# Kernel tuning notes

Hardware: AMD Instinct MI355X
Metric: run time of the kernel (lower is better)

Reference implementation:

```python
import jax, jax.numpy as jnp
import numpy as np

N = 500_000
E = 8_000_000
IN, HID, OUT = 1, 10, 4
BN_EPS = 1e-5


def _lin_init(key, fan_in, fan_out):
    kw, kb = jax.random.split(key)
    s = 1.0 / np.sqrt(fan_in)
    W = jax.random.uniform(kw, (fan_in, fan_out), minval=-s, maxval=s, dtype=jnp.float32)
    b = jax.random.uniform(kb, (fan_out,), minval=-s, maxval=s, dtype=jnp.float32)
    return W, b


def setup_inputs() -> dict:
    key = jax.random.key(0)
    ks = jax.random.split(key, 12)
    x = jax.random.normal(ks[0], (N, IN), dtype=jnp.float32)
    edge_index = jax.random.randint(ks[1], (2, E), 0, N, dtype=jnp.int64)
    edge_attr = jax.random.uniform(ks[2], (E,), dtype=jnp.float32)
    inp = {"x": x, "edge_index": edge_index, "edge_attr": edge_attr}
    dims = [(IN, HID), (HID, HID), (HID, HID)]
    for i, (di, do) in enumerate(dims, start=1):
        k1, k2 = jax.random.split(ks[2 + i])
        W1, b1 = _lin_init(k1, di, do)
        W2, b2 = _lin_init(k2, do, do)
        inp[f"W{i}a"], inp[f"b{i}a"] = W1, b1
        inp[f"W{i}b"], inp[f"b{i}b"] = W2, b2
        inp[f"g{i}"] = jnp.ones((do,), jnp.float32)
        inp[f"be{i}"] = jnp.zeros((do,), jnp.float32)
    Wf, bf = _lin_init(ks[10], 3 * HID, OUT)
    inp["Wf"], inp["bf"] = Wf, bf
    return inp


def _gin_layer(x, src, dst, Wa, ba, Wb, bb, g, be):
    # GINConv (eps=0): h_i = MLP(x_i + sum_{j->i} x_j); Linear->Linear->BatchNorm (train mode)
    agg = jax.ops.segment_sum(x[src], dst, num_segments=N)  # [N, d]
    h = x + agg
    h = h @ Wa + ba
    h = h @ Wb + bb
    mu = jnp.mean(h, axis=0)
    var = jnp.var(h, axis=0)
    return g * (h - mu) * jax.lax.rsqrt(var + BN_EPS) + be


def _modularity(s, src, dst, w):
    two_m = jnp.sum(w)
    pos = jnp.sum(w * jnp.sum(s[src] * s[dst], axis=-1)) / two_m
    deg = jax.ops.segment_sum(w, src, num_segments=N)  # [N]
    ds = (deg @ s) / two_m  # [OUT]
    return pos - jnp.sum(ds * ds)


def reference(x, edge_index, edge_attr,
              W1a, b1a, W1b, b1b, g1, be1,
              W2a, b2a, W2b, b2b, g2, be2,
              W3a, b3a, W3b, b3b, g3, be3,
              Wf, bf):
    src, dst = edge_index[0], edge_index[1]
    x11 = _gin_layer(x, src, dst, W1a, b1a, W1b, b1b, g1, be1)
    x12 = _gin_layer(x11, src, dst, W2a, b2a, W2b, b2b, g2, be2)
    x13 = _gin_layer(x12, src, dst, W3a, b3a, W3b, b3b, g3, be3)
    logits = jnp.concatenate([x11, x12, x13], axis=-1) @ Wf + bf
    s = jax.nn.softmax(logits, axis=-1)
    q = _modularity(s, src, dst, edge_attr)
    return s, q
```

## Files before the change

### kernel.cpp

```cpp
#include <hip/hip_runtime.h>
#include <hip/hip_bf16.h>

#define NN 500000
#define NE 8000000
#define NB 123
#define BSH 12
#define BSZ 4096
#define CAP 69632
#define M 8
#define NAGG (NB * M)
#define BN_EPS 1e-5f

typedef unsigned uv4 __attribute__((ext_vector_type(4)));
typedef float fv4 __attribute__((ext_vector_type(4)));
typedef unsigned long long u64;

__device__ __forceinline__ float waveReduceF(float v) {
#pragma unroll
    for (int o = 32; o > 0; o >>= 1) v += __shfl_down(v, o, 64);
    return v;
}
__device__ __forceinline__ double waveReduceD(double v) {
#pragma unroll
    for (int o = 32; o > 0; o >>= 1) v += __shfl_down(v, o, 64);
    return v;
}
__device__ __forceinline__ float u2f(unsigned short u) {
    return __bfloat162float(__builtin_bit_cast(__hip_bfloat16, u));
}
__device__ __forceinline__ unsigned short f2u(float f) {
    return __builtin_bit_cast(unsigned short, __float2bfloat16(f));
}
__device__ __forceinline__ u64 pk1(float v) {
    int iv = (int)rintf(v * 268435456.f);
    return ((u64)(long long)iv << 20) + 1ull;
}

__global__ void initk(int* __restrict__ cur)
{
    if (threadIdx.x < NB) cur[threadIdx.x] = (int)threadIdx.x * CAP;
}

__global__ __launch_bounds__(512) void scatterk(
    const int4* __restrict__ src4, const int4* __restrict__ dst4,
    const float4* __restrict__ w4, int* __restrict__ cur,
    unsigned* __restrict__ pairs, unsigned short* __restrict__ wp)
{
    __shared__ unsigned sEnt[4096];
    __shared__ unsigned short sW[4096];
    __shared__ unsigned char sB[4096];
    __shared__ int h[8][128];
    __shared__ int wOff[8][128];
    __shared__ int bOff[128];
    __shared__ int lb[128];
    __shared__ int tot[128];

    int tid = threadIdx.x, wv = tid >> 6;
    for (int j = tid; j < 8 * 128; j += 512) (&h[0][0])[j] = 0;
    __syncthreads();

    unsigned en[8]; unsigned short wb[8]; int rb[8];
#pragma unroll
    for (int k = 0; k < 2; k++) {
        int q = blockIdx.x * 1024 + k * 512 + tid;
        if (q < NE / 4) {
            int4 s4 = src4[q]; int4 d4 = dst4[q]; float4 ww = w4[q];
            int ss[4] = {s4.x, s4.y, s4.z, s4.w};
            int dd[4] = {d4.x, d4.y, d4.z, d4.w};
            float fw[4] = {ww.x, ww.y, ww.z, ww.w};
#pragma unroll
            for (int i = 0; i < 4; i++) {
                int d = dd[i], b = d >> BSH;
                en[k * 4 + i] = ((unsigned)(d & (BSZ - 1)) << 19) | (unsigned)ss[i];
                wb[k * 4 + i] = f2u(fw[i]);
                int rk = atomicAdd(&h[wv][b], 1);
                rb[k * 4 + i] = (rk << 8) | b;
            }
        } else {
#pragma unroll
            for (int i = 0; i < 4; i++) rb[k * 4 + i] = -1;
        }
    }
    __syncthreads();
    if (tid < NB) {
        int acc = 0;
#pragma unroll
        for (int w = 0; w < 8; w++) { wOff[w][tid] = acc; acc += h[w][tid]; }
        tot[tid] = acc;
        lb[tid] = atomicAdd(&cur[tid], acc);
    }
    __syncthreads();
    if (tid == 0) {
        int acc = 0;
        for (int b = 0; b < NB; b++) { bOff[b] = acc; acc += tot[b]; }
    }
    __syncthreads();
#pragma unroll
    for (int k = 0; k < 8; k++) {
        if (rb[k] >= 0) {
            int b = rb[k] & 255, rk = rb[k] >> 8;
            int pos = bOff[b] + wOff[wv][b] + rk;
            sEnt[pos] = en[k]; sW[pos] = wb[k]; sB[pos] = (unsigned char)b;
        }
    }
    __syncthreads();
    int nE = NE - blockIdx.x * 4096; if (nE > 4096) nE = 4096;
    for (int j = tid; j < nE; j += 512) {
        int b = sB[j];
        int glob = lb[b] + (j - bOff[b]);
        pairs[glob] = sEnt[j];
        wp[glob] = sW[j];
    }
}

__global__ __launch_bounds__(512) void agg1k(
    const unsigned* __restrict__ pairs, const int* __restrict__ cur,
    const float* __restrict__ x, u64* __restrict__ slab)
{
    __shared__ u64 t[BSZ];
    for (int j = threadIdx.x; j < BSZ; j += 512) t[j] = 0ull;
    __syncthreads();
    int B = blockIdx.x / M, sl = blockIdx.x % M;
    int b0 = B * CAP;
    int len = cur[B] - b0;
    int seg = (((len + M - 1) / M) + 3) & ~3;
    int lo = b0 + sl * seg;
    int hi = lo + seg, e1 = b0 + len;
    if (hi > e1) hi = e1;
    int n = hi - lo;
    if (n > 0) {
        int nq = n >> 2;
        const uv4* pq = (const uv4*)(pairs + lo);
        for (int i = threadIdx.x; i < nq; i += 1024) {
            uv4 pA = __builtin_nontemporal_load(pq + i);
            int iB = i + 512;
            bool vB = iB < nq;
            float a0 = x[pA.x & 524287u];
            float a1 = x[pA.y & 524287u];
            float a2 = x[pA.z & 524287u];
            float a3 = x[pA.w & 524287u];
            float c0, c1, c2, c3; unsigned d4, d5, d6, d7;
            if (vB) {
                uv4 pB = __builtin_nontemporal_load(pq + iB);
                c0 = x[pB.x & 524287u]; d4 = pB.x >> 19;
                c1 = x[pB.y & 524287u]; d5 = pB.y >> 19;
                c2 = x[pB.z & 524287u]; d6 = pB.z >> 19;
                c3 = x[pB.w & 524287u]; d7 = pB.w >> 19;
            }
            atomicAdd(&t[pA.x >> 19], pk1(a0));
            atomicAdd(&t[pA.y >> 19], pk1(a1));
            atomicAdd(&t[pA.z >> 19], pk1(a2));
            atomicAdd(&t[pA.w >> 19], pk1(a3));
            if (vB) {
                atomicAdd(&t[d4], pk1(c0));
                atomicAdd(&t[d5], pk1(c1));
                atomicAdd(&t[d6], pk1(c2));
                atomicAdd(&t[d7], pk1(c3));
            }
        }
        int rem = n & 3;
        if ((int)threadIdx.x < rem) {
            unsigned p = pairs[lo + (nq << 2) + threadIdx.x];
            atomicAdd(&t[p >> 19], pk1(x[p & 524287u]));
        }
    }
    __syncthreads();
    u64* sb = slab + (size_t)blockIdx.x * BSZ;
    for (int j = threadIdx.x; j < BSZ; j += 512)
        __builtin_nontemporal_store(t[j], sb + j);
}

__global__ __launch_bounds__(256) void mergeN1(
    const u64* __restrict__ slab, const float* __restrict__ x,
    float2* __restrict__ UN2, u64* __restrict__ ENC)
{
    int i = blockIdx.x * 256 + threadIdx.x;
    if (i >= NN) return;
    int B = i >> BSH, low = i & (BSZ - 1);
    u64 s = 0ull;
#pragma unroll
    for (int m = 0; m < M; m++)
        s += __builtin_nontemporal_load(slab + (size_t)(B * M + m) * BSZ + low);
    unsigned cn = (unsigned)(s & 0xFFFFFull);
    long long sv = (long long)(s - (u64)cn) >> 20;
    float u = x[i] + (float)((double)sv * 3.725290298461914e-09);
    UN2[i] = make_float2(u, (float)cn);
    long long iu = (long long)rintf(u * 67108864.f);
    ENC[i] = ((u64)iu << 22) + (u64)cn;
}

__global__ __launch_bounds__(512) void agg2k(
    const unsigned* __restrict__ pairs, const int* __restrict__ cur,
    const u64* __restrict__ ENC, u64* __restrict__ slab)
{
    __shared__ u64 t[BSZ];
    for (int j = threadIdx.x; j < BSZ; j += 512) t[j] = 0ull;
    __syncthreads();
    int B = blockIdx.x / M, sl = blockIdx.x % M;
    int b0 = B * CAP;
    int len = cur[B] - b0;
    int seg = (((len + M - 1) / M) + 3) & ~3;
    int lo = b0 + sl * seg;
    int hi = lo + seg, e1 = b0 + len;
    if (hi > e1) hi = e1;
    int n = hi - lo;
    if (n > 0) {
        int nq = n >> 2;
        const uv4* pq = (const uv4*)(pairs + lo);
        for (int i = threadIdx.x; i < nq; i += 1024) {
            uv4 pA = __builtin_nontemporal_load(pq + i);
            int iB = i + 512;
            bool vB = iB < nq;
            u64 e0 = ENC[pA.x & 524287u];
            u64 e1v = ENC[pA.y & 524287u];
            u64 e2 = ENC[pA.z & 524287u];
            u64 e3 = ENC[pA.w & 524287u];
            u64 e4, e5, e6, e7; unsigned d4, d5, d6, d7;
            if (vB) {
                uv4 pB = __builtin_nontemporal_load(pq + iB);
                e4 = ENC[pB.x & 524287u]; d4 = pB.x >> 19;
                e5 = ENC[pB.y & 524287u]; d5 = pB.y >> 19;
                e6 = ENC[pB.z & 524287u]; d6 = pB.z >> 19;
                e7 = ENC[pB.w & 524287u]; d7 = pB.w >> 19;
            }
            atomicAdd(&t[pA.x >> 19], e0);
            atomicAdd(&t[pA.y >> 19], e1v);
            atomicAdd(&t[pA.z >> 19], e2);
            atomicAdd(&t[pA.w >> 19], e3);
            if (vB) {
                atomicAdd(&t[d4], e4);
                atomicAdd(&t[d5], e5);
                atomicAdd(&t[d6], e6);
                atomicAdd(&t[d7], e7);
            }
        }
        int rem = n & 3;
        if ((int)threadIdx.x < rem) {
            unsigned p = pairs[lo + (nq << 2) + threadIdx.x];
            atomicAdd(&t[p >> 19], ENC[p & 524287u]);
        }
    }
    __syncthreads();
    u64* sb = slab + (size_t)blockIdx.x * BSZ;
    for (int j = threadIdx.x; j < BSZ; j += 512)
        __builtin_nontemporal_store(t[j], sb + j);
}

__global__ __launch_bounds__(256) void mergeN2(
    const u64* __restrict__ slab, float* __restrict__ SU, float* __restrict__ SN)
{
    int i = blockIdx.x * 256 + threadIdx.x;
    if (i >= NN) return;
    int B = i >> BSH, low = i & (BSZ - 1);
    u64 s = 0ull;
#pragma unroll
    for (int m = 0; m < M; m++)
        s += __builtin_nontemporal_load(slab + (size_t)(B * M + m) * BSZ + low);
    unsigned sn = (unsigned)(s & 0x3FFFFFull);
    long long sv = (long long)(s - (u64)sn) >> 22;
    float su = (float)((double)sv * 1.4901161193847656e-08);
    SU[i] = su;
    SN[i] = (float)sn;
}

__global__ __launch_bounds__(512) void agg3k(
    const unsigned* __restrict__ pairs, const int* __restrict__ cur,
    const float* __restrict__ SU, float* __restrict__ slab)
{
    __shared__ float t[BSZ];
    for (int j = threadIdx.x; j < BSZ; j += 512) t[j] = 0.f;
    __syncthreads();
    int B = blockIdx.x / M, sl = blockIdx.x % M;
    int b0 = B * CAP;
    int len = cur[B] - b0;
    int seg = (((len + M - 1) / M) + 3) & ~3;
    int lo = b0 + sl * seg;
    int hi = lo + seg, e1 = b0 + len;
    if (hi > e1) hi = e1;
    int n = hi - lo;
    if (n > 0) {
        int nq = n >> 2;
        const uv4* pq = (const uv4*)(pairs + lo);
        for (int i = threadIdx.x; i < nq; i += 1024) {
            uv4 pA = __builtin_nontemporal_load(pq + i);
            int iB = i + 512;
            bool vB = iB < nq;
            float a0 = SU[pA.x & 524287u];
            float a1 = SU[pA.y & 524287u];
            float a2 = SU[pA.z & 524287u];
            float a3 = SU[pA.w & 524287u];
            float c0, c1, c2, c3; unsigned d4, d5, d6, d7;
            if (vB) {
                uv4 pB = __builtin_nontemporal_load(pq + iB);
                c0 = SU[pB.x & 524287u]; d4 = pB.x >> 19;
                c1 = SU[pB.y & 524287u]; d5 = pB.y >> 19;
                c2 = SU[pB.z & 524287u]; d6 = pB.z >> 19;
                c3 = SU[pB.w & 524287u]; d7 = pB.w >> 19;
            }
            atomicAdd(&t[pA.x >> 19], a0);
            atomicAdd(&t[pA.y >> 19], a1);
            atomicAdd(&t[pA.z >> 19], a2);
            atomicAdd(&t[pA.w >> 19], a3);
            if (vB) {
                atomicAdd(&t[d4], c0);
                atomicAdd(&t[d5], c1);
                atomicAdd(&t[d6], c2);
                atomicAdd(&t[d7], c3);
            }
        }
        int rem = n & 3;
        if ((int)threadIdx.x < rem) {
            unsigned p = pairs[lo + (nq << 2) + threadIdx.x];
            atomicAdd(&t[p >> 19], SU[p & 524287u]);
        }
    }
    __syncthreads();
    float* sb = slab + (size_t)blockIdx.x * BSZ;
    for (int j = threadIdx.x; j < BSZ; j += 512)
        __builtin_nontemporal_store(t[j], sb + j);
}

__global__ __launch_bounds__(256) void m3mom(
    const float* __restrict__ slab, const float2* __restrict__ UN2,
    const float* __restrict__ SU, const float* __restrict__ SN,
    float* __restrict__ SSU, double* __restrict__ dm)
{
    int i = blockIdx.x * 256 + threadIdx.x;
    double z[5] = {0, 0, 0, 0, 0};
    if (i < NN) {
        int B = i >> BSH, low = i & (BSZ - 1);
        float ssu = 0.f;
#pragma unroll
        for (int m = 0; m < M; m++)
            ssu += __builtin_nontemporal_load(slab + (size_t)(B * M + m) * BSZ + low);
        SSU[i] = ssu;
        float2 un = UN2[i];
        z[0] = (double)un.x; z[1] = (double)un.y; z[2] = (double)SU[i];
        z[3] = (double)SN[i]; z[4] = (double)ssu;
    }
    double m[20];
#pragma unroll
    for (int a = 0; a < 5; a++) m[a] = z[a];
    int idx = 5;
#pragma unroll
    for (int a = 0; a < 5; a++)
#pragma unroll
        for (int b = a; b < 5; b++) m[idx++] = z[a] * z[b];

    __shared__ double part[4][20];
    int lane = threadIdx.x & 63, wid = threadIdx.x >> 6;
#pragma unroll
    for (int k = 0; k < 20; k++) {
        double r = waveReduceD(m[k]);
        if (lane == 0) part[wid][k] = r;
    }
    __syncthreads();
    if (threadIdx.x < 20)
        atomicAdd(&dm[threadIdx.x],
                  part[0][threadIdx.x] + part[1][threadIdx.x] +
                  part[2][threadIdx.x] + part[3][threadIdx.x]);
}

__device__ void mm1010(const float* in, const float* Wa, const float* Wb, float* out)
{
    float t[10];
    for (int m = 0; m < 10; m++) {
        float acc = 0.f;
        for (int k = 0; k < 10; k++) acc += in[k] * Wa[k * 10 + m];
        t[m] = acc;
    }
    for (int j = 0; j < 10; j++) {
        float acc = 0.f;
        for (int m = 0; m < 10; m++) acc += t[m] * Wb[m * 10 + j];
        out[j] = acc;
    }
}

__global__ void constk(
    const float* __restrict__ W1a, const float* __restrict__ b1a,
    const float* __restrict__ W1b, const float* __restrict__ b1b,
    const float* __restrict__ g1, const float* __restrict__ be1,
    const float* __restrict__ W2a, const float* __restrict__ b2a,
    const float* __restrict__ W2b, const float* __restrict__ b2b,
    const float* __restrict__ g2, const float* __restrict__ be2,
    const float* __restrict__ W3a, const float* __restrict__ b3a,
    const float* __restrict__ W3b, const float* __restrict__ b3b,
    const float* __restrict__ g3, const float* __restrict__ be3,
    const float* __restrict__ Wf, const float* __restrict__ bf_,
    const double* __restrict__ dm, float* __restrict__ Lout)
{
    if (threadIdx.x != 0 || blockIdx.x != 0) return;
    const double invN = 1.0 / (double)NN;
    double E[5];
    for (int m = 0; m < 5; m++) E[m] = dm[m] * invN;
    double C[5][5];
    {
        int idx = 5;
        for (int a = 0; a < 5; a++)
            for (int b = a; b < 5; b++) {
                double c = dm[idx++] * invN - E[a] * E[b];
                C[a][b] = c; C[b][a] = c;
            }
    }
    float v[10], c1[10];
    for (int j = 0; j < 10; j++) {
        float av = 0.f, ac = 0.f;
        for (int k = 0; k < 10; k++) {
            av += W1a[k] * W1b[k * 10 + j];
            ac += b1a[k] * W1b[k * 10 + j];
        }
        v[j] = av; c1[j] = ac + b1b[j];
    }
    double Eu = E[0], Vu = C[0][0];
    float p[10], q[10];
    for (int j = 0; j < 10; j++) {
        float var1 = (float)(Vu * (double)v[j] * (double)v[j]);
        float sc1 = g1[j] * rsqrtf(var1 + BN_EPS);
        p[j] = sc1 * v[j];
        q[j] = be1[j] - (float)Eu * p[j];
    }
    float r[10], s[10], d2[10];
    mm1010(p, W2a, W2b, r);
    mm1010(q, W2a, W2b, s);
    for (int j = 0; j < 10; j++) {
        float acc = b2b[j];
        for (int m = 0; m < 10; m++) acc += b2a[m] * W2b[m * 10 + j];
        d2[j] = acc;
    }
    double Ea = E[0] + E[2], Eb = 1.0 + E[1];
    double Va = C[0][0] + 2.0 * C[0][2] + C[2][2];
    double Vb = C[1][1];
    double Cab = C[0][1] + C[2][1];
    float rt[10], st[10], dt[10];
    for (int j = 0; j < 10; j++) {
        double rj = r[j], sj = s[j];
        float var2 = (float)(Va * rj * rj + Vb * sj * sj + 2.0 * Cab * rj * sj);
        float sc2 = g2[j] * rsqrtf(var2 + BN_EPS);
        rt[j] = sc2 * r[j];
        st[j] = sc2 * s[j];
        dt[j] = be2[j] - sc2 * (float)(Ea * rj + Eb * sj);
    }
    float r3[10], s3[10], t3[10], d3[10];
    mm1010(rt, W3a, W3b, r3);
    mm1010(st, W3a, W3b, s3);
    mm1010(dt, W3a, W3b, t3);
    for (int j = 0; j < 10; j++) {
        float acc = b3b[j];
        for (int m = 0; m < 10; m++) acc += b3a[m] * W3b[m * 10 + j];
        d3[j] = acc;
    }
    const double gA[5] = {1, 0, 2, 0, 1};
    const double gB[5] = {0, 2, 0, 1, 0};
    const double gC[5] = {0, 1, 0, 0, 0};
    double EA = E[0] + 2.0 * E[2] + E[4];
    double EB = 1.0 + 2.0 * E[1] + E[3];
    double EC = 1.0 + E[1];
    double VA = 0, VB = 0, VC = 0, CAB = 0, CAC = 0, CBC = 0;
    for (int a = 0; a < 5; a++)
        for (int b = 0; b < 5; b++) {
            double c = C[a][b];
            VA  += gA[a] * gA[b] * c;
            VB  += gB[a] * gB[b] * c;
            VC  += gC[a] * gC[b] * c;
            CAB += gA[a] * gB[b] * c;
            CAC += gA[a] * gC[b] * c;
            CBC += gB[a] * gC[b] * c;
        }
    float rh[10], sh[10], th[10], dh[10];
    for (int j = 0; j < 10; j++) {
        double rj = r3[j], sj = s3[j], tj = t3[j];
        float var3 = (float)(VA * rj * rj + VB * sj * sj + VC * tj * tj
                             + 2.0 * (CAB * rj * sj + CAC * rj * tj + CBC * sj * tj));
        float sc3 = g3[j] * rsqrtf(var3 + BN_EPS);
        rh[j] = sc3 * r3[j];
        sh[j] = sc3 * s3[j];
        th[j] = sc3 * t3[j];
        dh[j] = be3[j] - sc3 * (float)(EA * rj + EB * sj + EC * tj);
    }
    for (int k = 0; k < 4; k++) {
        float Lu = 0, Ln = 0, Lsu = 0, Lsn = 0, Lssu = 0, L0 = bf_[k];
        for (int j = 0; j < 10; j++) {
            float wf1 = Wf[j * 4 + k];
            float wf2 = Wf[(10 + j) * 4 + k];
            float wf3 = Wf[(20 + j) * 4 + k];
            Lu   += p[j] * wf1 + rt[j] * wf2 + rh[j] * wf3;
            Ln   += st[j] * wf2 + (2.f * sh[j] + th[j]) * wf3;
            Lsu  += rt[j] * wf2 + 2.f * rh[j] * wf3;
            Lsn  += sh[j] * wf3;
            Lssu += rh[j] * wf3;
            L0   += q[j] * wf1 + (st[j] + dt[j]) * wf2 + (sh[j] + th[j] + dh[j]) * wf3;
        }
        Lout[0 * 4 + k] = Lu;  Lout[1 * 4 + k] = Ln;   Lout[2 * 4 + k] = Lsu;
        Lout[3 * 4 + k] = Lsn; Lout[4 * 4 + k] = Lssu; Lout[5 * 4 + k] = L0;
    }
}

__global__ __launch_bounds__(256) void finalk(
    const float2* __restrict__ UN2, const float* __restrict__ SU,
    const float* __restrict__ SN, const float* __restrict__ SSU,
    const float* __restrict__ L,
    float4* __restrict__ sout, ushort4* __restrict__ sbf)
{
    __shared__ float sL[24];
    if (threadIdx.x < 24) sL[threadIdx.x] = L[threadIdx.x];
    __syncthreads();
    int i = blockIdx.x * 256 + threadIdx.x;
    if (i >= NN) return;
    float2 un = UN2[i];
    float u = un.x, n = un.y, su = SU[i], sn = SN[i], ssu = SSU[i];
    float lg[4];
#pragma unroll
    for (int k = 0; k < 4; k++)
        lg[k] = sL[k] * u + sL[4 + k] * n + sL[8 + k] * su
              + sL[12 + k] * sn + sL[16 + k] * ssu + sL[20 + k];
    float mx = fmaxf(fmaxf(lg[0], lg[1]), fmaxf(lg[2], lg[3]));
    float e0 = __expf(lg[0] - mx), e1 = __expf(lg[1] - mx);
    float e2 = __expf(lg[2] - mx), e3 = __expf(lg[3] - mx);
    float inv = 1.f / (e0 + e1 + e2 + e3);
    float s0 = e0 * inv, s1 = e1 * inv, s2 = e2 * inv, s3 = e3 * inv;
    fv4 o = {s0, s1, s2, s3};
    __builtin_nontemporal_store(o, (fv4*)sout + i);
    ushort4 pk; pk.x = f2u(s0); pk.y = f2u(s1); pk.z = f2u(s2); pk.w = f2u(s3);
    sbf[i] = pk;
}

__device__ __forceinline__ void modacc(u64 ua, u64 ub, float we, float* acc) {
    float ax = u2f((unsigned short)ua),         ay = u2f((unsigned short)(ua >> 16));
    float az = u2f((unsigned short)(ua >> 32)), aw = u2f((unsigned short)(ua >> 48));
    float bx = u2f((unsigned short)ub),         by = u2f((unsigned short)(ub >> 16));
    float bz = u2f((unsigned short)(ub >> 32)), bw = u2f((unsigned short)(ub >> 48));
    acc[0] += we;
    acc[1] += we * (ax * bx + ay * by + az * bz + aw * bw);
    acc[2] += we * ax; acc[3] += we * ay;
    acc[4] += we * az; acc[5] += we * aw;
}

__global__ __launch_bounds__(512) void modk(
    const unsigned* __restrict__ pairs, const unsigned short* __restrict__ wp,
    const int* __restrict__ cur, const u64* __restrict__ sbfU,
    float* __restrict__ scal)
{
    __shared__ u64 sS[BSZ];
    int B = blockIdx.x / M, sl = blockIdx.x % M;
    for (int j = threadIdx.x; j < BSZ; j += 512) {
        int g = (B << BSH) + j;
        sS[j] = (g < NN) ? sbfU[g] : 0ull;
    }
    __syncthreads();
    int b0 = B * CAP;
    int len = cur[B] - b0;
    int seg = (((len + M - 1) / M) + 3) & ~3;
    int lo = b0 + sl * seg;
    int hi = lo + seg, e1 = b0 + len;
    if (hi > e1) hi = e1;
    int n = hi - lo;
    float acc[6] = {0, 0, 0, 0, 0, 0};
    if (n > 0) {
        int nq = n >> 2;
        const uv4* pq = (const uv4*)(pairs + lo);
        const u64* wq = (const u64*)(wp + lo);
        for (int i = threadIdx.x; i < nq; i += 1024) {
            uv4 pA = __builtin_nontemporal_load(pq + i);
            u64 wA = __builtin_nontemporal_load(wq + i);
            int iB = i + 512;
            bool vB = iB < nq;
            u64 a0 = sbfU[pA.x & 524287u];
            u64 a1 = sbfU[pA.y & 524287u];
            u64 a2 = sbfU[pA.z & 524287u];
            u64 a3 = sbfU[pA.w & 524287u];
            uv4 pB; u64 wB; u64 a4, a5, a6, a7;
            if (vB) {
                pB = __builtin_nontemporal_load(pq + iB);
                wB = __builtin_nontemporal_load(wq + iB);
                a4 = sbfU[pB.x & 524287u];
                a5 = sbfU[pB.y & 524287u];
                a6 = sbfU[pB.z & 524287u];
                a7 = sbfU[pB.w & 524287u];
            }
            modacc(a0, sS[pA.x >> 19], u2f((unsigned short)wA),         acc);
            modacc(a1, sS[pA.y >> 19], u2f((unsigned short)(wA >> 16)), acc);
            modacc(a2, sS[pA.z >> 19], u2f((unsigned short)(wA >> 32)), acc);
            modacc(a3, sS[pA.w >> 19], u2f((unsigned short)(wA >> 48)), acc);
            if (vB) {
                modacc(a4, sS[pB.x >> 19], u2f((unsigned short)wB),         acc);
                modacc(a5, sS[pB.y >> 19], u2f((unsigned short)(wB >> 16)), acc);
                modacc(a6, sS[pB.z >> 19], u2f((unsigned short)(wB >> 32)), acc);
                modacc(a7, sS[pB.w >> 19], u2f((unsigned short)(wB >> 48)), acc);
            }
        }
        int rem = n & 3;
        if ((int)threadIdx.x < rem) {
            int idx = lo + (nq << 2) + threadIdx.x;
            unsigned p = pairs[idx];
            modacc(sbfU[p & 524287u], sS[p >> 19], u2f(wp[idx]), acc);
        }
    }
    __shared__ float part[8][6];
    int lane = threadIdx.x & 63, wid = threadIdx.x >> 6;
#pragma unroll
    for (int k = 0; k < 6; k++) {
        float r = waveReduceF(acc[k]);
        if (lane == 0) part[wid][k] = r;
    }
    __syncthreads();
    if (threadIdx.x < 6) {
        float vsum = 0.f;
#pragma unroll
        for (int wdi = 0; wdi < 8; wdi++) vsum += part[wdi][threadIdx.x];
        int off = (threadIdx.x == 0) ? 128 : (threadIdx.x == 1 ? 129 : 130 + threadIdx.x);
        atomicAdd(&scal[off], vsum);
    }
}

__global__ void qk(const float* __restrict__ scal, float* __restrict__ out)
{
    if (threadIdx.x == 0) {
        float inv = 1.f / scal[128];
        float posv = scal[129] * inv;
        float acc = 0.f;
#pragma unroll
        for (int k = 0; k < 4; k++) {
            float d = scal[132 + k] * inv;
            acc += d * d;
        }
        out[(size_t)NN * 4] = posv - acc;
    }
}

extern "C" void kernel_launch(void* const* d_in, const int* in_sizes, int n_in,
                              void* d_out, int out_size, void* d_ws, size_t ws_size,
                              hipStream_t stream) {
    const float* x  = (const float*)d_in[0];
    const int*  ei  = (const int*)d_in[1];
    const int*  src = ei;
    const int*  dst = ei + NE;
    const float* w   = (const float*)d_in[2];
    const float* W1a = (const float*)d_in[3];  const float* b1a = (const float*)d_in[4];
    const float* W1b = (const float*)d_in[5];  const float* b1b = (const float*)d_in[6];
    const float* g1  = (const float*)d_in[7];  const float* be1 = (const float*)d_in[8];
    const float* W2a = (const float*)d_in[9];  const float* b2a = (const float*)d_in[10];
    const float* W2b = (const float*)d_in[11]; const float* b2b = (const float*)d_in[12];
    const float* g2  = (const float*)d_in[13]; const float* be2 = (const float*)d_in[14];
    const float* W3a = (const float*)d_in[15]; const float* b3a = (const float*)d_in[16];
    const float* W3b = (const float*)d_in[17]; const float* b3b = (const float*)d_in[18];
    const float* g3  = (const float*)d_in[19]; const float* be3 = (const float*)d_in[20];
    const float* Wf  = (const float*)d_in[21]; const float* bfb = (const float*)d_in[22];

    float*  sc   = (float*)d_ws;
    int*    sci  = (int*)d_ws;
    double* dm   = (double*)(sc + 384);
    unsigned* pairs = (unsigned*)(sc + 1024);
    unsigned short* wp = (unsigned short*)(pairs + (size_t)NB * CAP);
    float*  slab = (float*)(wp + (size_t)NB * CAP);
    u64*    slabU = (u64*)slab;
    float2* UN2  = (float2*)(slab + (size_t)NAGG * 2 * BSZ);
    float*  SU   = (float*)(UN2 + NN);
    float*  SN   = SU + NN;
    float*  SSU  = SN + NN;
    ushort4* sbf = (ushort4*)(SSU + NN);
    u64*    ENC  = (u64*)(sbf + NN);
    float*  sout = (float*)d_out;

    const int NB_N  = (NN + 255) / 256;
    const int NB_EQ = (NE / 4 + 1023) / 1024;

    hipMemsetAsync(sc, 0, 4096, stream);
    initk<<<1, 128, 0, stream>>>(sci + 832);

    scatterk<<<NB_EQ, 512, 0, stream>>>((const int4*)src, (const int4*)dst,
                                        (const float4*)w, sci + 832, pairs, wp);

    agg1k<<<NAGG, 512, 0, stream>>>(pairs, sci + 832, x, slabU);
    mergeN1<<<NB_N, 256, 0, stream>>>(slabU, x, UN2, ENC);
    agg2k<<<NAGG, 512, 0, stream>>>(pairs, sci + 832, ENC, slabU);
    mergeN2<<<NB_N, 256, 0, stream>>>(slabU, SU, SN);
    agg3k<<<NAGG, 512, 0, stream>>>(pairs, sci + 832, SU, slab);
    m3mom<<<NB_N, 256, 0, stream>>>(slab, UN2, SU, SN, SSU, dm);

    constk<<<1, 64, 0, stream>>>(W1a, b1a, W1b, b1b, g1, be1,
                                 W2a, b2a, W2b, b2b, g2, be2,
                                 W3a, b3a, W3b, b3b, g3, be3,
                                 Wf, bfb, dm, sc + 160);
    finalk<<<NB_N, 256, 0, stream>>>(UN2, SU, SN, SSU, sc + 160, (float4*)sout, sbf);
    modk<<<NAGG, 512, 0, stream>>>(pairs, wp, sci + 832, (const u64*)sbf, sc);
    qk<<<1, 64, 0, stream>>>(sc, sout);
}
```

Before: 496.6 us.

## Deepen gather unrolling, fold tiny kernels into last-block epilogues, nontemporal scatter

```diff
diff --git a/kernel.cpp b/kernel.cpp
--- a/kernel.cpp
+++ b/kernel.cpp
@@ -12,6 +12,7 @@
 #define BN_EPS 1e-5f
 
 typedef unsigned uv4 __attribute__((ext_vector_type(4)));
+typedef int iv4 __attribute__((ext_vector_type(4)));
 typedef float fv4 __attribute__((ext_vector_type(4)));
 typedef unsigned long long u64;
 
@@ -36,14 +37,9 @@
     return ((u64)(long long)iv << 20) + 1ull;
 }
 
-__global__ void initk(int* __restrict__ cur)
-{
-    if (threadIdx.x < NB) cur[threadIdx.x] = (int)threadIdx.x * CAP;
-}
-
 __global__ __launch_bounds__(512) void scatterk(
-    const int4* __restrict__ src4, const int4* __restrict__ dst4,
-    const float4* __restrict__ w4, int* __restrict__ cur,
+    const iv4* __restrict__ src4, const iv4* __restrict__ dst4,
+    const fv4* __restrict__ w4, int* __restrict__ cur,
     unsigned* __restrict__ pairs, unsigned short* __restrict__ wp)
 {
     __shared__ unsigned sEnt[4096];
@@ -64,7 +60,9 @@
     for (int k = 0; k < 2; k++) {
         int q = blockIdx.x * 1024 + k * 512 + tid;
         if (q < NE / 4) {
-            int4 s4 = src4[q]; int4 d4 = dst4[q]; float4 ww = w4[q];
+            iv4 s4 = __builtin_nontemporal_load(src4 + q);
+            iv4 d4 = __builtin_nontemporal_load(dst4 + q);
+            fv4 ww = __builtin_nontemporal_load(w4 + q);
             int ss[4] = {s4.x, s4.y, s4.z, s4.w};
             int dd[4] = {d4.x, d4.y, d4.z, d4.w};
             float fw[4] = {ww.x, ww.y, ww.z, ww.w};
@@ -87,12 +85,22 @@
 #pragma unroll
         for (int w = 0; w < 8; w++) { wOff[w][tid] = acc; acc += h[w][tid]; }
         tot[tid] = acc;
-        lb[tid] = atomicAdd(&cur[tid], acc);
-    }
-    __syncthreads();
-    if (tid == 0) {
-        int acc = 0;
-        for (int b = 0; b < NB; b++) { bOff[b] = acc; acc += tot[b]; }
+        lb[tid] = tid * CAP + atomicAdd(&cur[tid], acc);
+    }
+    __syncthreads();
+    if (tid < 64) {
+        int lane = tid;
+        int a = (2 * lane < NB) ? tot[2 * lane] : 0;
+        int b = (2 * lane + 1 < NB) ? tot[2 * lane + 1] : 0;
+        int s = a + b;
+#pragma unroll
+        for (int o = 1; o < 64; o <<= 1) {
+            int t = __shfl_up(s, o, 64);
+            if (lane >= o) s += t;
+        }
+        int excl = s - (a + b);
+        bOff[2 * lane] = excl;
+        bOff[2 * lane + 1] = excl + a;
     }
     __syncthreads();
 #pragma unroll
@@ -108,8 +116,8 @@
     for (int j = tid; j < nE; j += 512) {
         int b = sB[j];
         int glob = lb[b] + (j - bOff[b]);
-        pairs[glob] = sEnt[j];
-        wp[glob] = sW[j];
+        __builtin_nontemporal_store(sEnt[j], pairs + glob);
+        __builtin_nontemporal_store(sW[j], wp + glob);
     }
 }
 
@@ -122,7 +130,7 @@
     __syncthreads();
     int B = blockIdx.x / M, sl = blockIdx.x % M;
     int b0 = B * CAP;
-    int len = cur[B] - b0;
+    int len = cur[B];
     int seg = (((len + M - 1) / M) + 3) & ~3;
     int lo = b0 + sl * seg;
     int hi = lo + seg, e1 = b0 + len;
@@ -131,31 +139,51 @@
     if (n > 0) {
         int nq = n >> 2;
         const uv4* pq = (const uv4*)(pairs + lo);
-        for (int i = threadIdx.x; i < nq; i += 1024) {
-            uv4 pA = __builtin_nontemporal_load(pq + i);
-            int iB = i + 512;
-            bool vB = iB < nq;
-            float a0 = x[pA.x & 524287u];
-            float a1 = x[pA.y & 524287u];
-            float a2 = x[pA.z & 524287u];
-            float a3 = x[pA.w & 524287u];
-            float c0, c1, c2, c3; unsigned d4, d5, d6, d7;
-            if (vB) {
-                uv4 pB = __builtin_nontemporal_load(pq + iB);
-                c0 = x[pB.x & 524287u]; d4 = pB.x >> 19;
-                c1 = x[pB.y & 524287u]; d5 = pB.y >> 19;
-                c2 = x[pB.z & 524287u]; d6 = pB.z >> 19;
-                c3 = x[pB.w & 524287u]; d7 = pB.w >> 19;
-            }
-            atomicAdd(&t[pA.x >> 19], pk1(a0));
-            atomicAdd(&t[pA.y >> 19], pk1(a1));
-            atomicAdd(&t[pA.z >> 19], pk1(a2));
-            atomicAdd(&t[pA.w >> 19], pk1(a3));
-            if (vB) {
-                atomicAdd(&t[d4], pk1(c0));
-                atomicAdd(&t[d5], pk1(c1));
-                atomicAdd(&t[d6], pk1(c2));
-                atomicAdd(&t[d7], pk1(c3));
+        for (int i = threadIdx.x; i < nq; i += 2048) {
+            int i1 = i + 512, i2 = i + 1024, i3 = i + 1536;
+            bool v1 = i1 < nq, v2 = i2 < nq, v3 = i3 < nq;
+            uv4 p0 = __builtin_nontemporal_load(pq + i);
+            uv4 p1, p2, p3;
+            if (v1) p1 = __builtin_nontemporal_load(pq + i1);
+            if (v2) p2 = __builtin_nontemporal_load(pq + i2);
+            if (v3) p3 = __builtin_nontemporal_load(pq + i3);
+            float a0 = x[p0.x & 524287u], a1 = x[p0.y & 524287u];
+            float a2 = x[p0.z & 524287u], a3 = x[p0.w & 524287u];
+            float b0v, b1v, b2v, b3v, c0, c1, c2, c3, d0, d1, d2, d3;
+            if (v1) {
+                b0v = x[p1.x & 524287u]; b1v = x[p1.y & 524287u];
+                b2v = x[p1.z & 524287u]; b3v = x[p1.w & 524287u];
+            }
+            if (v2) {
+                c0 = x[p2.x & 524287u]; c1 = x[p2.y & 524287u];
+                c2 = x[p2.z & 524287u]; c3 = x[p2.w & 524287u];
+            }
+            if (v3) {
+                d0 = x[p3.x & 524287u]; d1 = x[p3.y & 524287u];
+                d2 = x[p3.z & 524287u]; d3 = x[p3.w & 524287u];
+            }
+            __builtin_amdgcn_sched_barrier(0);
+            atomicAdd(&t[p0.x >> 19], pk1(a0));
+            atomicAdd(&t[p0.y >> 19], pk1(a1));
+            atomicAdd(&t[p0.z >> 19], pk1(a2));
+            atomicAdd(&t[p0.w >> 19], pk1(a3));
+            if (v1) {
+                atomicAdd(&t[p1.x >> 19], pk1(b0v));
+                atomicAdd(&t[p1.y >> 19], pk1(b1v));
+                atomicAdd(&t[p1.z >> 19], pk1(b2v));
+                atomicAdd(&t[p1.w >> 19], pk1(b3v));
+            }
+            if (v2) {
+                atomicAdd(&t[p2.x >> 19], pk1(c0));
+                atomicAdd(&t[p2.y >> 19], pk1(c1));
+                atomicAdd(&t[p2.z >> 19], pk1(c2));
+                atomicAdd(&t[p2.w >> 19], pk1(c3));
+            }
+            if (v3) {
+                atomicAdd(&t[p3.x >> 19], pk1(d0));
+                atomicAdd(&t[p3.y >> 19], pk1(d1));
+                atomicAdd(&t[p3.z >> 19], pk1(d2));
+                atomicAdd(&t[p3.w >> 19], pk1(d3));
             }
         }
         int rem = n & 3;
@@ -198,7 +226,7 @@
     __syncthreads();
     int B = blockIdx.x / M, sl = blockIdx.x % M;
     int b0 = B * CAP;
-    int len = cur[B] - b0;
+    int len = cur[B];
     int seg = (((len + M - 1) / M) + 3) & ~3;
     int lo = b0 + sl * seg;
     int hi = lo + seg, e1 = b0 + len;
@@ -207,31 +235,40 @@
     if (n > 0) {
         int nq = n >> 2;
         const uv4* pq = (const uv4*)(pairs + lo);
-        for (int i = threadIdx.x; i < nq; i += 1024) {
-            uv4 pA = __builtin_nontemporal_load(pq + i);
-            int iB = i + 512;
-            bool vB = iB < nq;
-            u64 e0 = ENC[pA.x & 524287u];
-            u64 e1v = ENC[pA.y & 524287u];
-            u64 e2 = ENC[pA.z & 524287u];
-            u64 e3 = ENC[pA.w & 524287u];
-            u64 e4, e5, e6, e7; unsigned d4, d5, d6, d7;
-            if (vB) {
-                uv4 pB = __builtin_nontemporal_load(pq + iB);
-                e4 = ENC[pB.x & 524287u]; d4 = pB.x >> 19;
-                e5 = ENC[pB.y & 524287u]; d5 = pB.y >> 19;
-                e6 = ENC[pB.z & 524287u]; d6 = pB.z >> 19;
-                e7 = ENC[pB.w & 524287u]; d7 = pB.w >> 19;
-            }
-            atomicAdd(&t[pA.x >> 19], e0);
-            atomicAdd(&t[pA.y >> 19], e1v);
-            atomicAdd(&t[pA.z >> 19], e2);
-            atomicAdd(&t[pA.w >> 19], e3);
-            if (vB) {
-                atomicAdd(&t[d4], e4);
-                atomicAdd(&t[d5], e5);
-                atomicAdd(&t[d6], e6);
-                atomicAdd(&t[d7], e7);
+        for (int i = threadIdx.x; i < nq; i += 1536) {
+            int i1 = i + 512, i2 = i + 1024;
+            bool v1 = i1 < nq, v2 = i2 < nq;
+            uv4 p0 = __builtin_nontemporal_load(pq + i);
+            uv4 p1, p2;
+            if (v1) p1 = __builtin_nontemporal_load(pq + i1);
+            if (v2) p2 = __builtin_nontemporal_load(pq + i2);
+            u64 e0 = ENC[p0.x & 524287u], e1v = ENC[p0.y & 524287u];
+            u64 e2 = ENC[p0.z & 524287u], e3 = ENC[p0.w & 524287u];
+            u64 f0, f1, f2, f3, g0, g1, g2, g3;
+            if (v1) {
+                f0 = ENC[p1.x & 524287u]; f1 = ENC[p1.y & 524287u];
+                f2 = ENC[p1.z & 524287u]; f3 = ENC[p1.w & 524287u];
+            }
+            if (v2) {
+                g0 = ENC[p2.x & 524287u]; g1 = ENC[p2.y & 524287u];
+                g2 = ENC[p2.z & 524287u]; g3 = ENC[p2.w & 524287u];
+            }
+            __builtin_amdgcn_sched_barrier(0);
+            atomicAdd(&t[p0.x >> 19], e0);
+            atomicAdd(&t[p0.y >> 19], e1v);
+            atomicAdd(&t[p0.z >> 19], e2);
+            atomicAdd(&t[p0.w >> 19], e3);
+            if (v1) {
+                atomicAdd(&t[p1.x >> 19], f0);
+                atomicAdd(&t[p1.y >> 19], f1);
+                atomicAdd(&t[p1.z >> 19], f2);
+                atomicAdd(&t[p1.w >> 19], f3);
+            }
+            if (v2) {
+                atomicAdd(&t[p2.x >> 19], g0);
+                atomicAdd(&t[p2.y >> 19], g1);
+                atomicAdd(&t[p2.z >> 19], g2);
+                atomicAdd(&t[p2.w >> 19], g3);
             }
         }
         int rem = n & 3;
@@ -272,7 +309,7 @@
     __syncthreads();
     int B = blockIdx.x / M, sl = blockIdx.x % M;
     int b0 = B * CAP;
-    int len = cur[B] - b0;
+    int len = cur[B];
     int seg = (((len + M - 1) / M) + 3) & ~3;
     int lo = b0 + sl * seg;
     int hi = lo + seg, e1 = b0 + len;
@@ -281,31 +318,51 @@
     if (n > 0) {
         int nq = n >> 2;
         const uv4* pq = (const uv4*)(pairs + lo);
-        for (int i = threadIdx.x; i < nq; i += 1024) {
-            uv4 pA = __builtin_nontemporal_load(pq + i);
-            int iB = i + 512;
-            bool vB = iB < nq;
-            float a0 = SU[pA.x & 524287u];
-            float a1 = SU[pA.y & 524287u];
-            float a2 = SU[pA.z & 524287u];
-            float a3 = SU[pA.w & 524287u];
-            float c0, c1, c2, c3; unsigned d4, d5, d6, d7;
-            if (vB) {
-                uv4 pB = __builtin_nontemporal_load(pq + iB);
-                c0 = SU[pB.x & 524287u]; d4 = pB.x >> 19;
-                c1 = SU[pB.y & 524287u]; d5 = pB.y >> 19;
-                c2 = SU[pB.z & 524287u]; d6 = pB.z >> 19;
-                c3 = SU[pB.w & 524287u]; d7 = pB.w >> 19;
-            }
-            atomicAdd(&t[pA.x >> 19], a0);
-            atomicAdd(&t[pA.y >> 19], a1);
-            atomicAdd(&t[pA.z >> 19], a2);
-            atomicAdd(&t[pA.w >> 19], a3);
-            if (vB) {
-                atomicAdd(&t[d4], c0);
-                atomicAdd(&t[d5], c1);
-                atomicAdd(&t[d6], c2);
-                atomicAdd(&t[d7], c3);
+        for (int i = threadIdx.x; i < nq; i += 2048) {
+            int i1 = i + 512, i2 = i + 1024, i3 = i + 1536;
+            bool v1 = i1 < nq, v2 = i2 < nq, v3 = i3 < nq;
+            uv4 p0 = __builtin_nontemporal_load(pq + i);
+            uv4 p1, p2, p3;
+            if (v1) p1 = __builtin_nontemporal_load(pq + i1);
+            if (v2) p2 = __builtin_nontemporal_load(pq + i2);
+            if (v3) p3 = __builtin_nontemporal_load(pq + i3);
+            float a0 = SU[p0.x & 524287u], a1 = SU[p0.y & 524287u];
+            float a2 = SU[p0.z & 524287u], a3 = SU[p0.w & 524287u];
+            float b0v, b1v, b2v, b3v, c0, c1, c2, c3, d0, d1, d2, d3;
+            if (v1) {
+                b0v = SU[p1.x & 524287u]; b1v = SU[p1.y & 524287u];
+                b2v = SU[p1.z & 524287u]; b3v = SU[p1.w & 524287u];
+            }
+            if (v2) {
+                c0 = SU[p2.x & 524287u]; c1 = SU[p2.y & 524287u];
+                c2 = SU[p2.z & 524287u]; c3 = SU[p2.w & 524287u];
+            }
+            if (v3) {
+                d0 = SU[p3.x & 524287u]; d1 = SU[p3.y & 524287u];
+                d2 = SU[p3.z & 524287u]; d3 = SU[p3.w & 524287u];
+            }
+            __builtin_amdgcn_sched_barrier(0);
+            atomicAdd(&t[p0.x >> 19], a0);
+            atomicAdd(&t[p0.y >> 19], a1);
+            atomicAdd(&t[p0.z >> 19], a2);
+            atomicAdd(&t[p0.w >> 19], a3);
+            if (v1) {
+                atomicAdd(&t[p1.x >> 19], b0v);
+                atomicAdd(&t[p1.y >> 19], b1v);
+                atomicAdd(&t[p1.z >> 19], b2v);
+                atomicAdd(&t[p1.w >> 19], b3v);
+            }
+            if (v2) {
+                atomicAdd(&t[p2.x >> 19], c0);
+                atomicAdd(&t[p2.y >> 19], c1);
+                atomicAdd(&t[p2.z >> 19], c2);
+                atomicAdd(&t[p2.w >> 19], c3);
+            }
+            if (v3) {
+                atomicAdd(&t[p3.x >> 19], d0);
+                atomicAdd(&t[p3.y >> 19], d1);
+                atomicAdd(&t[p3.z >> 19], d2);
+                atomicAdd(&t[p3.w >> 19], d3);
             }
         }
         int rem = n & 3;
@@ -318,47 +375,6 @@
     float* sb = slab + (size_t)blockIdx.x * BSZ;
     for (int j = threadIdx.x; j < BSZ; j += 512)
         __builtin_nontemporal_store(t[j], sb + j);
-}
-
-__global__ __launch_bounds__(256) void m3mom(
-    const float* __restrict__ slab, const float2* __restrict__ UN2,
-    const float* __restrict__ SU, const float* __restrict__ SN,
-    float* __restrict__ SSU, double* __restrict__ dm)
-{
-    int i = blockIdx.x * 256 + threadIdx.x;
-    double z[5] = {0, 0, 0, 0, 0};
-    if (i < NN) {
-        int B = i >> BSH, low = i & (BSZ - 1);
-        float ssu = 0.f;
-#pragma unroll
-        for (int m = 0; m < M; m++)
-            ssu += __builtin_nontemporal_load(slab + (size_t)(B * M + m) * BSZ + low);
-        SSU[i] = ssu;
-        float2 un = UN2[i];
-        z[0] = (double)un.x; z[1] = (double)un.y; z[2] = (double)SU[i];
-        z[3] = (double)SN[i]; z[4] = (double)ssu;
-    }
-    double m[20];
-#pragma unroll
-    for (int a = 0; a < 5; a++) m[a] = z[a];
-    int idx = 5;
-#pragma unroll
-    for (int a = 0; a < 5; a++)
-#pragma unroll
-        for (int b = a; b < 5; b++) m[idx++] = z[a] * z[b];
-
-    __shared__ double part[4][20];
-    int lane = threadIdx.x & 63, wid = threadIdx.x >> 6;
-#pragma unroll
-    for (int k = 0; k < 20; k++) {
-        double r = waveReduceD(m[k]);
-        if (lane == 0) part[wid][k] = r;
-    }
-    __syncthreads();
-    if (threadIdx.x < 20)
-        atomicAdd(&dm[threadIdx.x],
-                  part[0][threadIdx.x] + part[1][threadIdx.x] +
-                  part[2][threadIdx.x] + part[3][threadIdx.x]);
 }
 
 __device__ void mm1010(const float* in, const float* Wa, const float* Wb, float* out)
@@ -376,29 +392,25 @@
     }
 }
 
-__global__ void constk(
-    const float* __restrict__ W1a, const float* __restrict__ b1a,
-    const float* __restrict__ W1b, const float* __restrict__ b1b,
-    const float* __restrict__ g1, const float* __restrict__ be1,
-    const float* __restrict__ W2a, const float* __restrict__ b2a,
-    const float* __restrict__ W2b, const float* __restrict__ b2b,
-    const float* __restrict__ g2, const float* __restrict__ be2,
-    const float* __restrict__ W3a, const float* __restrict__ b3a,
-    const float* __restrict__ W3b, const float* __restrict__ b3b,
-    const float* __restrict__ g3, const float* __restrict__ be3,
-    const float* __restrict__ Wf, const float* __restrict__ bf_,
-    const double* __restrict__ dm, float* __restrict__ Lout)
-{
-    if (threadIdx.x != 0 || blockIdx.x != 0) return;
+__device__ void constBody(
+    const float* W1a, const float* b1a, const float* W1b, const float* b1b,
+    const float* g1, const float* be1,
+    const float* W2a, const float* b2a, const float* W2b, const float* b2b,
+    const float* g2, const float* be2,
+    const float* W3a, const float* b3a, const float* W3b, const float* b3b,
+    const float* g3, const float* be3,
+    const float* Wf, const float* bf_,
+    const double* dmv, float* Lout)
+{
     const double invN = 1.0 / (double)NN;
     double E[5];
-    for (int m = 0; m < 5; m++) E[m] = dm[m] * invN;
+    for (int m = 0; m < 5; m++) E[m] = dmv[m] * invN;
     double C[5][5];
     {
         int idx = 5;
         for (int a = 0; a < 5; a++)
             for (int b = a; b < 5; b++) {
-                double c = dm[idx++] * invN - E[a] * E[b];
+                double c = dmv[idx++] * invN - E[a] * E[b];
                 C[a][b] = c; C[b][a] = c;
             }
     }
@@ -495,6 +507,72 @@
     }
 }
 
+__global__ __launch_bounds__(256) void m3momC(
+    const float* __restrict__ slab, const float2* __restrict__ UN2,
+    const float* __restrict__ SU, const float* __restrict__ SN,
+    float* __restrict__ SSU, double* __restrict__ dm, int* __restrict__ cnt,
+    const float* __restrict__ W1a, const float* __restrict__ b1a,
+    const float* __restrict__ W1b, const float* __restrict__ b1b,
+    const float* __restrict__ g1, const float* __restrict__ be1,
+    const float* __restrict__ W2a, const float* __restrict__ b2a,
+    const float* __restrict__ W2b, const float* __restrict__ b2b,
+    const float* __restrict__ g2, const float* __restrict__ be2,
+    const float* __restrict__ W3a, const float* __restrict__ b3a,
+    const float* __restrict__ W3b, const float* __restrict__ b3b,
+    const float* __restrict__ g3, const float* __restrict__ be3,
+    const float* __restrict__ Wf, const float* __restrict__ bf_,
+    float* __restrict__ Lout)
+{
+    int i = blockIdx.x * 256 + threadIdx.x;
+    double z[5] = {0, 0, 0, 0, 0};
+    if (i < NN) {
+        int B = i >> BSH, low = i & (BSZ - 1);
+        float ssu = 0.f;
+#pragma unroll
+        for (int m = 0; m < M; m++)
+            ssu += __builtin_nontemporal_load(slab + (size_t)(B * M + m) * BSZ + low);
+        SSU[i] = ssu;
+        float2 un = UN2[i];
+        z[0] = (double)un.x; z[1] = (double)un.y; z[2] = (double)SU[i];
+        z[3] = (double)SN[i]; z[4] = (double)ssu;
+    }
+    double m[20];
+#pragma unroll
+    for (int a = 0; a < 5; a++) m[a] = z[a];
+    int idx = 5;
+#pragma unroll
+    for (int a = 0; a < 5; a++)
+#pragma unroll
+        for (int b = a; b < 5; b++) m[idx++] = z[a] * z[b];
+
+    __shared__ double part[4][20];
+    int lane = threadIdx.x & 63, wid = threadIdx.x >> 6;
+#pragma unroll
+    for (int k = 0; k < 20; k++) {
+        double r = waveReduceD(m[k]);
+        if (lane == 0) part[wid][k] = r;
+    }
+    __syncthreads();
+    if (threadIdx.x < 20) {
+        atomicAdd(&dm[threadIdx.x],
+                  part[0][threadIdx.x] + part[1][threadIdx.x] +
+                  part[2][threadIdx.x] + part[3][threadIdx.x]);
+        __threadfence();
+    }
+    __syncthreads();
+    if (threadIdx.x == 0) {
+        if (atomicAdd(cnt, 1) == (int)gridDim.x - 1) {
+            double dmv[20];
+#pragma unroll
+            for (int k = 0; k < 20; k++) dmv[k] = atomicAdd(&dm[k], 0.0);
+            constBody(W1a, b1a, W1b, b1b, g1, be1,
+                      W2a, b2a, W2b, b2b, g2, be2,
+                      W3a, b3a, W3b, b3b, g3, be3,
+                      Wf, bf_, dmv, Lout);
+        }
+    }
+}
+
 __global__ __launch_bounds__(256) void finalk(
     const float2* __restrict__ UN2, const float* __restrict__ SU,
     const float* __restrict__ SN, const float* __restrict__ SSU,
@@ -535,10 +613,10 @@
     acc[4] += we * az; acc[5] += we * aw;
 }
 
-__global__ __launch_bounds__(512) void modk(
+__global__ __launch_bounds__(512) void modkQ(
     const unsigned* __restrict__ pairs, const unsigned short* __restrict__ wp,
     const int* __restrict__ cur, const u64* __restrict__ sbfU,
-    float* __restrict__ scal)
+    float* __restrict__ scal, int* __restrict__ cnt, float* __restrict__ outq)
 {
     __shared__ u64 sS[BSZ];
     int B = blockIdx.x / M, sl = blockIdx.x % M;
@@ -548,7 +626,7 @@
     }
     __syncthreads();
     int b0 = B * CAP;
-    int len = cur[B] - b0;
+    int len = cur[B];
     int seg = (((len + M - 1) / M) + 3) & ~3;
     int lo = b0 + sl * seg;
     int hi = lo + seg, e1 = b0 + len;
@@ -559,33 +637,43 @@
         int nq = n >> 2;
         const uv4* pq = (const uv4*)(pairs + lo);
         const u64* wq = (const u64*)(wp + lo);
-        for (int i = threadIdx.x; i < nq; i += 1024) {
-            uv4 pA = __builtin_nontemporal_load(pq + i);
-            u64 wA = __builtin_nontemporal_load(wq + i);
-            int iB = i + 512;
-            bool vB = iB < nq;
-            u64 a0 = sbfU[pA.x & 524287u];
-            u64 a1 = sbfU[pA.y & 524287u];
-            u64 a2 = sbfU[pA.z & 524287u];
-            u64 a3 = sbfU[pA.w & 524287u];
-            uv4 pB; u64 wB; u64 a4, a5, a6, a7;
-            if (vB) {
-                pB = __builtin_nontemporal_load(pq + iB);
-                wB = __builtin_nontemporal_load(wq + iB);
-                a4 = sbfU[pB.x & 524287u];
-                a5 = sbfU[pB.y & 524287u];
-                a6 = sbfU[pB.z & 524287u];
-                a7 = sbfU[pB.w & 524287u];
-            }
-            modacc(a0, sS[pA.x >> 19], u2f((unsigned short)wA),         acc);
-            modacc(a1, sS[pA.y >> 19], u2f((unsigned short)(wA >> 16)), acc);
-            modacc(a2, sS[pA.z >> 19], u2f((unsigned short)(wA >> 32)), acc);
-            modacc(a3, sS[pA.w >> 19], u2f((unsigned short)(wA >> 48)), acc);
-            if (vB) {
-                modacc(a4, sS[pB.x >> 19], u2f((unsigned short)wB),         acc);
-                modacc(a5, sS[pB.y >> 19], u2f((unsigned short)(wB >> 16)), acc);
-                modacc(a6, sS[pB.z >> 19], u2f((unsigned short)(wB >> 32)), acc);
-                modacc(a7, sS[pB.w >> 19], u2f((unsigned short)(wB >> 48)), acc);
+        for (int i = threadIdx.x; i < nq; i += 1536) {
+            int i1 = i + 512, i2 = i + 1024;
+            bool v1 = i1 < nq, v2 = i2 < nq;
+            uv4 p0 = __builtin_nontemporal_load(pq + i);
+            u64 w0 = __builtin_nontemporal_load(wq + i);
+            uv4 p1, p2; u64 w1, w2;
+            if (v1) { p1 = __builtin_nontemporal_load(pq + i1);
+                      w1 = __builtin_nontemporal_load(wq + i1); }
+            if (v2) { p2 = __builtin_nontemporal_load(pq + i2);
+                      w2 = __builtin_nontemporal_load(wq + i2); }
+            u64 a0 = sbfU[p0.x & 524287u], a1 = sbfU[p0.y & 524287u];
+            u64 a2 = sbfU[p0.z & 524287u], a3 = sbfU[p0.w & 524287u];
+            u64 b0v, b1v, b2v, b3v, c0, c1, c2, c3;
+            if (v1) {
+                b0v = sbfU[p1.x & 524287u]; b1v = sbfU[p1.y & 524287u];
+                b2v = sbfU[p1.z & 524287u]; b3v = sbfU[p1.w & 524287u];
+            }
+            if (v2) {
+                c0 = sbfU[p2.x & 524287u]; c1 = sbfU[p2.y & 524287u];
+                c2 = sbfU[p2.z & 524287u]; c3 = sbfU[p2.w & 524287u];
+            }
+            __builtin_amdgcn_sched_barrier(0);
+            modacc(a0, sS[p0.x >> 19], u2f((unsigned short)w0),         acc);
+            modacc(a1, sS[p0.y >> 19], u2f((unsigned short)(w0 >> 16)), acc);
+            modacc(a2, sS[p0.z >> 19], u2f((unsigned short)(w0 >> 32)), acc);
+            modacc(a3, sS[p0.w >> 19], u2f((unsigned short)(w0 >> 48)), acc);
+            if (v1) {
+                modacc(b0v, sS[p1.x >> 19], u2f((unsigned short)w1),         acc);
+                modacc(b1v, sS[p1.y >> 19], u2f((unsigned short)(w1 >> 16)), acc);
+                modacc(b2v, sS[p1.z >> 19], u2f((unsigned short)(w1 >> 32)), acc);
+                modacc(b3v, sS[p1.w >> 19], u2f((unsigned short)(w1 >> 48)), acc);
+            }
+            if (v2) {
+                modacc(c0, sS[p2.x >> 19], u2f((unsigned short)w2),         acc);
+                modacc(c1, sS[p2.y >> 19], u2f((unsigned short)(w2 >> 16)), acc);
+                modacc(c2, sS[p2.z >> 19], u2f((unsigned short)(w2 >> 32)), acc);
+                modacc(c3, sS[p2.w >> 19], u2f((unsigned short)(w2 >> 48)), acc);
             }
         }
         int rem = n & 3;
@@ -609,21 +697,23 @@
         for (int wdi = 0; wdi < 8; wdi++) vsum += part[wdi][threadIdx.x];
         int off = (threadIdx.x == 0) ? 128 : (threadIdx.x == 1 ? 129 : 130 + threadIdx.x);
         atomicAdd(&scal[off], vsum);
-    }
-}
-
-__global__ void qk(const float* __restrict__ scal, float* __restrict__ out)
-{
+        __threadfence();
+    }
+    __syncthreads();
     if (threadIdx.x == 0) {
-        float inv = 1.f / scal[128];
-        float posv = scal[129] * inv;
-        float acc = 0.f;
-#pragma unroll
-        for (int k = 0; k < 4; k++) {
-            float d = scal[132 + k] * inv;
-            acc += d * d;
-        }
-        out[(size_t)NN * 4] = posv - acc;
+        if (atomicAdd(cnt, 1) == (int)gridDim.x - 1) {
+            float tm = atomicAdd(&scal[128], 0.f);
+            float pos = atomicAdd(&scal[129], 0.f);
+            float inv = 1.f / tm;
+            float posv = pos * inv;
+            float acq = 0.f;
+#pragma unroll
+            for (int k = 0; k < 4; k++) {
+                float d = atomicAdd(&scal[132 + k], 0.f) * inv;
+                acq += d * d;
+            }
+            outq[(size_t)NN * 4] = posv - acq;
+        }
     }
 }
 
@@ -665,23 +755,22 @@
     const int NB_EQ = (NE / 4 + 1023) / 1024;
 
     hipMemsetAsync(sc, 0, 4096, stream);
-    initk<<<1, 128, 0, stream>>>(sci + 832);
-
-    scatterk<<<NB_EQ, 512, 0, stream>>>((const int4*)src, (const int4*)dst,
-                                        (const float4*)w, sci + 832, pairs, wp);
+
+    scatterk<<<NB_EQ, 512, 0, stream>>>((const iv4*)src, (const iv4*)dst,
+                                        (const fv4*)w, sci + 832, pairs, wp);
 
     agg1k<<<NAGG, 512, 0, stream>>>(pairs, sci + 832, x, slabU);
     mergeN1<<<NB_N, 256, 0, stream>>>(slabU, x, UN2, ENC);
     agg2k<<<NAGG, 512, 0, stream>>>(pairs, sci + 832, ENC, slabU);
     mergeN2<<<NB_N, 256, 0, stream>>>(slabU, SU, SN);
     agg3k<<<NAGG, 512, 0, stream>>>(pairs, sci + 832, SU, slab);
-    m3mom<<<NB_N, 256, 0, stream>>>(slab, UN2, SU, SN, SSU, dm);
-
-    constk<<<1, 64, 0, stream>>>(W1a, b1a, W1b, b1b, g1, be1,
-                                 W2a, b2a, W2b, b2b, g2, be2,
-                                 W3a, b3a, W3b, b3b, g3, be3,
-                                 Wf, bfb, dm, sc + 160);
+    m3momC<<<NB_N, 256, 0, stream>>>(slab, UN2, SU, SN, SSU, dm, sci + 960,
+                                     W1a, b1a, W1b, b1b, g1, be1,
+                                     W2a, b2a, W2b, b2b, g2, be2,
+                                     W3a, b3a, W3b, b3b, g3, be3,
+                                     Wf, bfb, sc + 160);
+
     finalk<<<NB_N, 256, 0, stream>>>(UN2, SU, SN, SSU, sc + 160, (float4*)sout, sbf);
-    modk<<<NAGG, 512, 0, stream>>>(pairs, wp, sci + 832, (const u64*)sbf, sc);
-    qk<<<1, 64, 0, stream>>>(sc, sout);
-}
+    modkQ<<<NAGG, 512, 0, stream>>>(pairs, wp, sci + 832, (const u64*)sbf, sc,
+                                    sci + 961, sout);
+}
```

Measured after the change: 553.6 us. +11.5%, slower.
